# Kernel optimization log

Hardware: AMD Instinct MI355X
Metric: run time of the kernel (lower is better)

## Reference

```python
import jax, jax.numpy as jnp
import numpy as np

N, E = 20000, 320000
EPS = 1e-5
NEG_SLOPE = 0.2


def gat_conv(x, src, dst, W, att_src, att_dst, bias, num_nodes):
    # W: [Fin, H*C], att_*: [H, C], bias: [H*C]
    H, C = att_src.shape
    h = (x @ W).reshape(num_nodes, H, C)            # [N,H,C]
    a_s = jnp.einsum('nhc,hc->nh', h, att_src)      # [N,H]
    a_d = jnp.einsum('nhc,hc->nh', h, att_dst)      # [N,H]
    e = jax.nn.leaky_relu(a_s[src] + a_d[dst], NEG_SLOPE)  # [E,H]
    m = jax.ops.segment_max(e, dst, num_segments=num_nodes)       # per-dst max (self-loops guarantee non-empty)
    ex = jnp.exp(e - m[dst])
    s = jax.ops.segment_sum(ex, dst, num_segments=num_nodes)
    alpha = ex / s[dst]                              # [E,H] segment softmax
    out = jax.ops.segment_sum(h[src] * alpha[:, :, None], dst, num_segments=num_nodes)  # [N,H,C]
    return out.reshape(num_nodes, H * C) + bias


def batch_norm(x, gamma, beta):
    mu = x.mean(axis=0)
    var = x.var(axis=0)  # biased, as torch BN uses for normalization
    return (x - mu) * jax.lax.rsqrt(var + EPS) * gamma + beta


def setup_inputs() -> dict:
    key = jax.random.key(0)
    ks = jax.random.split(key, 32)
    x = jax.random.normal(ks[0], (N, 512), dtype=jnp.float32)
    edge_index = jax.random.randint(ks[1], (2, E), 0, N, dtype=jnp.int32)
    d = {"x": x, "edge_index": edge_index}
    # layer configs: (Fin, C_out, H)
    cfgs = [(512, 64, 8), (512, 64, 4), (256, 64, 2), (128, 16, 1)]
    i = 2
    for li, (fin, c, h) in enumerate(cfgs, start=1):
        sc = 1.0 / np.sqrt(fin)
        d[f"W{li}"] = jax.random.normal(ks[i], (fin, h * c), dtype=jnp.float32) * sc; i += 1
        d[f"as{li}"] = jax.random.normal(ks[i], (h, c), dtype=jnp.float32) * 0.1; i += 1
        d[f"ad{li}"] = jax.random.normal(ks[i], (h, c), dtype=jnp.float32) * 0.1; i += 1
        d[f"b{li}"] = jnp.zeros((h * c,), dtype=jnp.float32)
        if li < 4:
            d[f"g{li}"] = jnp.ones((h * c,), dtype=jnp.float32)
            d[f"be{li}"] = jnp.zeros((h * c,), dtype=jnp.float32)
    return d


def reference(x, edge_index, W1, as1, ad1, b1, g1, be1, W2, as2, ad2, b2, g2, be2, W3, as3, ad3, b3, g3, be3, W4, as4, ad4, b4):
    num_nodes = x.shape[0]
    loop = jnp.arange(num_nodes, dtype=edge_index.dtype)
    src = jnp.concatenate([edge_index[0], loop])  # add_self_loops=True
    dst = jnp.concatenate([edge_index[1], loop])
    h = gat_conv(x, src, dst, W1, as1, ad1, b1, num_nodes)
    h = jax.nn.elu(batch_norm(h, g1, be1))
    h = gat_conv(h, src, dst, W2, as2, ad2, b2, num_nodes)
    h = jax.nn.elu(batch_norm(h, g2, be2))
    h = gat_conv(h, src, dst, W3, as3, ad3, b3, num_nodes)
    h = jax.nn.elu(batch_norm(h, g3, be3))
    h = gat_conv(h, src, dst, W4, as4, ad4, b4, num_nodes)
    return jax.nn.log_softmax(h, axis=1)
```

## Files before the change

### kernel.cpp

```cpp
#include <hip/hip_runtime.h>
#include <hip/hip_bf16.h>
#include <cstdint>
#include <cstddef>

#define NN 20000
#define EE 320000
#define ET (EE + NN)
#define MPAD 20096
#define BNP 256

typedef __attribute__((ext_vector_type(8))) short  short8;
typedef __attribute__((ext_vector_type(4))) float  floatx4;

__device__ inline unsigned short f2bf(float f) {
    unsigned u = __float_as_uint(f);
    u += 0x7FFFu + ((u >> 16) & 1u);
    return (unsigned short)(u >> 16);
}
__device__ inline float bf2f(unsigned short b) {
    return __uint_as_float(((unsigned)b) << 16);
}
__device__ inline float bflo(unsigned u) { return __uint_as_float(u << 16); }
__device__ inline float bfhi(unsigned u) { return __uint_as_float(u & 0xFFFF0000u); }

template <int H> struct VecT;
template <> struct VecT<8> { using T = uint4; };
template <> struct VecT<4> { using T = uint2; };
template <> struct VecT<2> { using T = unsigned; };

__global__ void zero_i32(int* __restrict__ p, int n) {
    int i = blockIdx.x * blockDim.x + threadIdx.x;
    if (i < n) p[i] = 0;
}

__global__ void cvt_a_bf16(const float* __restrict__ in, unsigned short* __restrict__ out,
                           int M, int Mpad, int K) {
    long long base = ((long long)blockIdx.x * blockDim.x + threadIdx.x) * 4;
    if (base >= (long long)Mpad * K) return;
    int row = (int)(base / K);
    float4 v = make_float4(0.f, 0.f, 0.f, 0.f);
    if (row < M) v = *(const float4*)(in + base);
    ushort4 o;
    o.x = f2bf(v.x); o.y = f2bf(v.y); o.z = f2bf(v.z); o.w = f2bf(v.w);
    *(ushort4*)(out + base) = o;
}

__global__ void cvt_w_t(const float* __restrict__ W, unsigned short* __restrict__ Wt,
                        int K, int N) {
    int i = blockIdx.x * blockDim.x + threadIdx.x;
    if (i >= K * N) return;
    int k = i / N, n = i - k * N;
    Wt[(size_t)n * K + k] = f2bf(W[i]);
}

__global__ void count_edges(const int* __restrict__ dst, int* __restrict__ cnt) {
    int e = blockIdx.x * blockDim.x + threadIdx.x;
    if (e >= ET) return;
    int d = (e < EE) ? dst[e] : (e - EE);
    atomicAdd(&cnt[d], 1);
}

__global__ void scan20k(const int* __restrict__ cnt, int* __restrict__ rowp,
                        int* __restrict__ wptr, int n) {
    __shared__ int sd[1024];
    __shared__ int run;
    int t = threadIdx.x;
    if (t == 0) run = 0;
    __syncthreads();
    for (int base = 0; base < n; base += 1024) {
        int i = base + t;
        int v = (i < n) ? cnt[i] : 0;
        sd[t] = v;
        __syncthreads();
        for (int o = 1; o < 1024; o <<= 1) {
            int u = (t >= o) ? sd[t - o] : 0;
            __syncthreads();
            sd[t] += u;
            __syncthreads();
        }
        int incl = sd[t];
        int excl = incl - v;
        if (i < n) { int rp = run + excl; rowp[i] = rp; wptr[i] = rp; }
        __syncthreads();
        if (t == 1023) run += sd[1023];
        __syncthreads();
    }
    if (t == 0) rowp[n] = run;
}

__global__ void fill_edges(const int* __restrict__ src, const int* __restrict__ dst,
                           int* __restrict__ wptr, int* __restrict__ colx) {
    int e = blockIdx.x * blockDim.x + threadIdx.x;
    if (e >= ET) return;
    int s, d;
    if (e < EE) { s = src[e]; d = dst[e]; } else { s = e - EE; d = e - EE; }
    int pos = atomicAdd(&wptr[d], 1);
    colx[pos] = s;
}

__global__ __launch_bounds__(256) void gemm_bf16_fused(
        const unsigned short* __restrict__ A, const unsigned short* __restrict__ Bt,
        unsigned short* __restrict__ hN, float* __restrict__ aS, float* __restrict__ aD,
        const float* __restrict__ atts, const float* __restrict__ attd,
        int M, int N, int K) {
    __shared__ unsigned short As[128][40];
    __shared__ unsigned short Bs[128][40];
    const int t = threadIdx.x;
    const int lane = t & 63, wave = t >> 6;
    const int wm = wave >> 1, wn = wave & 1;
    const int quad = lane >> 4, mrow = lane & 15;
    const int row0 = blockIdx.y * 128, col0 = blockIdx.x * 128;
    const int srow = t >> 2, schunk = (t & 3) * 8;
    const int H = N >> 6;

    floatx4 acc[4][4];
#pragma unroll
    for (int i = 0; i < 4; ++i)
#pragma unroll
        for (int j = 0; j < 4; ++j)
#pragma unroll
            for (int r = 0; r < 4; ++r) acc[i][j][r] = 0.f;

    for (int k0 = 0; k0 < K; k0 += 32) {
        uint4 ra0 = *(const uint4*)(A  + (size_t)(row0 + srow)      * K + k0 + schunk);
        uint4 ra1 = *(const uint4*)(A  + (size_t)(row0 + srow + 64) * K + k0 + schunk);
        uint4 rb0 = *(const uint4*)(Bt + (size_t)(col0 + srow)      * K + k0 + schunk);
        uint4 rb1 = *(const uint4*)(Bt + (size_t)(col0 + srow + 64) * K + k0 + schunk);
        __syncthreads();
        *(uint4*)&As[srow][schunk]      = ra0;
        *(uint4*)&As[srow + 64][schunk] = ra1;
        *(uint4*)&Bs[srow][schunk]      = rb0;
        *(uint4*)&Bs[srow + 64][schunk] = rb1;
        __syncthreads();

        short8 af[4], bfr[4];
#pragma unroll
        for (int i = 0; i < 4; ++i)
            af[i] = *(const short8*)&As[wm * 64 + i * 16 + mrow][quad * 8];
#pragma unroll
        for (int j = 0; j < 4; ++j)
            bfr[j] = *(const short8*)&Bs[wn * 64 + j * 16 + mrow][quad * 8];
#pragma unroll
        for (int i = 0; i < 4; ++i)
#pragma unroll
            for (int j = 0; j < 4; ++j)
                acc[i][j] = __builtin_amdgcn_mfma_f32_16x16x32_bf16(af[i], bfr[j], acc[i][j], 0, 0, 0);
    }

    const int head = (col0 + wn * 64) >> 6;
    float attS[4], attD[4];
#pragma unroll
    for (int j = 0; j < 4; ++j) {
        attS[j] = atts[head * 64 + j * 16 + mrow];
        attD[j] = attd[head * 64 + j * 16 + mrow];
    }

#pragma unroll
    for (int i = 0; i < 4; ++i) {
#pragma unroll
        for (int r = 0; r < 4; ++r) {
            int row = row0 + wm * 64 + i * 16 + quad * 4 + r;
            float ps = acc[i][0][r] * attS[0] + acc[i][1][r] * attS[1]
                     + acc[i][2][r] * attS[2] + acc[i][3][r] * attS[3];
            float pd = acc[i][0][r] * attD[0] + acc[i][1][r] * attD[1]
                     + acc[i][2][r] * attD[2] + acc[i][3][r] * attD[3];
#pragma unroll
            for (int o = 1; o < 16; o <<= 1) {
                ps += __shfl_xor(ps, o);
                pd += __shfl_xor(pd, o);
            }
            if (row < M) {
                if (mrow == 0) {
                    aS[(size_t)row * H + head] = ps;
                    aD[(size_t)row * H + head] = pd;
                }
#pragma unroll
                for (int j = 0; j < 4; ++j)
                    hN[(size_t)row * N + col0 + wn * 64 + j * 16 + mrow] = f2bf(acc[i][j][r]);
            }
        }
    }
}

template <int H>
__global__ __launch_bounds__(256) void gat_agg_all(
        const unsigned short* __restrict__ hN,
        const float* __restrict__ aS, const float* __restrict__ aD,
        const int* __restrict__ rowp, const int* __restrict__ colx,
        const float* __restrict__ bias, float* __restrict__ out, int Nn) {
    constexpr int F = H * 64;
    using V = typename VecT<H>::T;
    __shared__ float pbuf[4][64 * H];
    __shared__ int   snbuf[4][64];
    const int wave = threadIdx.x >> 6, lane = threadIdx.x & 63;
    const int n = blockIdx.x * 4 + wave;
    if (n >= Nn) return;
    const int hd = (lane * H) >> 6;
    const int chbase = lane * H;

    const int b0 = rowp[n], b1 = rowp[n + 1];

    float adv[H];
#pragma unroll
    for (int h = 0; h < H; ++h) adv[h] = aD[(size_t)n * H + h];

    float m[H], s[H];
#pragma unroll
    for (int h = 0; h < H; ++h) { m[h] = -1e30f; s[h] = 0.f; }
    for (int c0 = b0; c0 < b1; c0 += 64) {
        int cnt = min(64, b1 - c0);
        float e[H];
#pragma unroll
        for (int h = 0; h < H; ++h) e[h] = -1e30f;
        if (lane < cnt) {
            int sn = colx[c0 + lane];
#pragma unroll
            for (int h = 0; h < H; ++h) {
                float tt = aS[(size_t)sn * H + h] + adv[h];
                e[h] = (tt > 0.f) ? tt : 0.2f * tt;
            }
        }
#pragma unroll
        for (int h = 0; h < H; ++h) {
            float mc = e[h];
#pragma unroll
            for (int o = 32; o > 0; o >>= 1) mc = fmaxf(mc, __shfl_xor(mc, o));
            float nm = fmaxf(m[h], mc);
            s[h] *= __expf(m[h] - nm);
            float p = (lane < cnt) ? __expf(e[h] - nm) : 0.f;
#pragma unroll
            for (int o = 32; o > 0; o >>= 1) p += __shfl_xor(p, o);
            s[h] += p; m[h] = nm;
        }
    }
    float inv[H];
#pragma unroll
    for (int h = 0; h < H; ++h) inv[h] = 1.f / s[h];

    float acc[H];
#pragma unroll
    for (int h = 0; h < H; ++h) acc[h] = 0.f;

    for (int c0 = b0; c0 < b1; c0 += 64) {
        int cnt = min(64, b1 - c0);
        if (lane < cnt) {
            int sn = colx[c0 + lane];
            snbuf[wave][lane] = sn;
#pragma unroll
            for (int h = 0; h < H; ++h) {
                float tt = aS[(size_t)sn * H + h] + adv[h];
                tt = (tt > 0.f) ? tt : 0.2f * tt;
                pbuf[wave][lane * H + h] = __expf(tt - m[h]) * inv[h];
            }
        }
        __threadfence_block();

        int j = 0;
        for (; j + 4 <= cnt; j += 4) {
            int s0 = snbuf[wave][j],     s1 = snbuf[wave][j + 1];
            int s2 = snbuf[wave][j + 2], s3 = snbuf[wave][j + 3];
            float p0 = pbuf[wave][(j + 0) * H + hd];
            float p1 = pbuf[wave][(j + 1) * H + hd];
            float p2 = pbuf[wave][(j + 2) * H + hd];
            float p3 = pbuf[wave][(j + 3) * H + hd];
            V q0 = *(const V*)(hN + (size_t)s0 * F + chbase);
            V q1 = *(const V*)(hN + (size_t)s1 * F + chbase);
            V q2 = *(const V*)(hN + (size_t)s2 * F + chbase);
            V q3 = *(const V*)(hN + (size_t)s3 * F + chbase);
            const unsigned* u0 = (const unsigned*)&q0;
            const unsigned* u1 = (const unsigned*)&q1;
            const unsigned* u2 = (const unsigned*)&q2;
            const unsigned* u3 = (const unsigned*)&q3;
#pragma unroll
            for (int k = 0; k < H / 2; ++k) {
                acc[2 * k]     += p0 * bflo(u0[k]) + p1 * bflo(u1[k]) + p2 * bflo(u2[k]) + p3 * bflo(u3[k]);
                acc[2 * k + 1] += p0 * bfhi(u0[k]) + p1 * bfhi(u1[k]) + p2 * bfhi(u2[k]) + p3 * bfhi(u3[k]);
            }
        }
        for (; j < cnt; ++j) {
            int sj = snbuf[wave][j];
            float pj = pbuf[wave][j * H + hd];
            V q = *(const V*)(hN + (size_t)sj * F + chbase);
            const unsigned* u = (const unsigned*)&q;
#pragma unroll
            for (int k = 0; k < H / 2; ++k) {
                acc[2 * k]     += pj * bflo(u[k]);
                acc[2 * k + 1] += pj * bfhi(u[k]);
            }
        }
        __threadfence_block();
    }

#pragma unroll
    for (int h = 0; h < H; ++h)
        out[(size_t)n * F + chbase + h] = acc[h] + bias[chbase + h];
}

__global__ __launch_bounds__(256) void gemm_l4_fused(const unsigned short* __restrict__ A,
                                                     const float* __restrict__ B,
                                                     unsigned short* __restrict__ C,
                                                     float* __restrict__ aS, float* __restrict__ aD,
                                                     const float* __restrict__ atts,
                                                     const float* __restrict__ attd,
                                                     int M, int N, int K) {
    __shared__ float As[16][65];
    __shared__ float Bs[16][64];
    const int tid = threadIdx.x;
    const int tx = tid & 15, ty = tid >> 4;
    const int row0 = blockIdx.y * 64, col0 = blockIdx.x * 64;
    const int rA = tid >> 2, kq = (tid & 3) << 2;
    const int rB = tid >> 4, cq = (tid & 15) << 2;
    float acc[4][4] = {};

    for (int k0 = 0; k0 < K; k0 += 16) {
        ushort4 ha = *(const ushort4*)(A + (size_t)(row0 + rA) * K + k0 + kq);
        float4 fb = make_float4(0.f, 0.f, 0.f, 0.f);
        int bcol = col0 + cq;
        if (bcol < N) fb = *(const float4*)(B + (size_t)(k0 + rB) * N + bcol);
        As[kq + 0][rA] = bf2f(ha.x); As[kq + 1][rA] = bf2f(ha.y);
        As[kq + 2][rA] = bf2f(ha.z); As[kq + 3][rA] = bf2f(ha.w);
        *(float4*)&Bs[rB][cq] = fb;
        __syncthreads();
#pragma unroll
        for (int k = 0; k < 16; ++k) {
            float a0 = As[k][ty * 4 + 0];
            float a1 = As[k][ty * 4 + 1];
            float a2 = As[k][ty * 4 + 2];
            float a3 = As[k][ty * 4 + 3];
            float4 b = *(float4*)&Bs[k][tx * 4];
            acc[0][0] += a0 * b.x; acc[0][1] += a0 * b.y; acc[0][2] += a0 * b.z; acc[0][3] += a0 * b.w;
            acc[1][0] += a1 * b.x; acc[1][1] += a1 * b.y; acc[1][2] += a1 * b.z; acc[1][3] += a1 * b.w;
            acc[2][0] += a2 * b.x; acc[2][1] += a2 * b.y; acc[2][2] += a2 * b.z; acc[2][3] += a2 * b.w;
            acc[3][0] += a3 * b.x; acc[3][1] += a3 * b.y; acc[3][2] += a3 * b.z; acc[3][3] += a3 * b.w;
        }
        __syncthreads();
    }
    float as_part[4], ad_part[4];
#pragma unroll
    for (int i = 0; i < 4; ++i) { as_part[i] = 0.f; ad_part[i] = 0.f; }
    if (tx < 4) {
#pragma unroll
        for (int i = 0; i < 4; ++i) {
#pragma unroll
            for (int jj = 0; jj < 4; ++jj) {
                int c = tx * 4 + jj;
                as_part[i] += acc[i][jj] * atts[c];
                ad_part[i] += acc[i][jj] * attd[c];
            }
        }
    }
#pragma unroll
    for (int i = 0; i < 4; ++i) {
        float ps = as_part[i], pd = ad_part[i];
        ps += __shfl_xor(ps, 1); ps += __shfl_xor(ps, 2);
        pd += __shfl_xor(pd, 1); pd += __shfl_xor(pd, 2);
        int r = row0 + ty * 4 + i;
        if (r < M) {
            if (tx == 0) { aS[r] = ps; aD[r] = pd; }
#pragma unroll
            for (int jj = 0; jj < 4; ++jj) {
                int c = col0 + tx * 4 + jj;
                if (c < N) C[(size_t)r * N + c] = f2bf(acc[i][jj]);
            }
        }
    }
}

template <int C>
__global__ void gat_agg_l4_ls(const unsigned short* __restrict__ ht,
                              const float* __restrict__ as, const float* __restrict__ aD,
                              const int* __restrict__ rowp, const int* __restrict__ colx,
                              const float* __restrict__ bias, float* __restrict__ out, int Nn) {
    int n = blockIdx.x * 4 + (threadIdx.x >> 6);
    int lane = threadIdx.x & 63;
    if (n >= Nn) return;
    float adv = aD[n];
    int b0 = rowp[n], b1 = rowp[n + 1];

    float m = -1e30f, s = 0.f, acc = 0.f;
    for (int c0 = b0; c0 < b1; c0 += 64) {
        int cnt = b1 - c0; if (cnt > 64) cnt = 64;
        int sn = 0; float e = -1e30f;
        if (lane < cnt) {
            sn = colx[c0 + lane];
            float tt = as[sn] + adv;
            e = (tt > 0.f) ? tt : 0.2f * tt;
        }
        float mc = e;
#pragma unroll
        for (int o = 32; o > 0; o >>= 1) mc = fmaxf(mc, __shfl_xor(mc, o));
        float nm = fmaxf(m, mc);
        float sc = __expf(m - nm);
        acc *= sc; s *= sc;
        float p = (lane < cnt) ? __expf(e - nm) : 0.f;
        float ps = p;
#pragma unroll
        for (int o = 32; o > 0; o >>= 1) ps += __shfl_xor(ps, o);
        s += ps; m = nm;

        int j = 0;
        for (; j + 4 <= cnt; j += 4) {
            int s0 = __shfl(sn, j),     s1 = __shfl(sn, j + 1);
            int s2 = __shfl(sn, j + 2), s3 = __shfl(sn, j + 3);
            float p0 = __shfl(p, j),     p1 = __shfl(p, j + 1);
            float p2 = __shfl(p, j + 2), p3 = __shfl(p, j + 3);
            float h0 = 0.f, h1 = 0.f, h2 = 0.f, h3 = 0.f;
            if (lane < C) {
                h0 = bf2f(ht[(size_t)s0 * C + lane]);
                h1 = bf2f(ht[(size_t)s1 * C + lane]);
                h2 = bf2f(ht[(size_t)s2 * C + lane]);
                h3 = bf2f(ht[(size_t)s3 * C + lane]);
            }
            acc += p0 * h0 + p1 * h1 + p2 * h2 + p3 * h3;
        }
        for (; j < cnt; ++j) {
            int sj = __shfl(sn, j);
            float pj = __shfl(p, j);
            float hv = (lane < C) ? bf2f(ht[(size_t)sj * C + lane]) : 0.f;
            acc += pj * hv;
        }
    }
    float v = (lane < C) ? (acc / s + bias[lane]) : -1e30f;
    float mx = v;
#pragma unroll
    for (int o = 8; o > 0; o >>= 1) mx = fmaxf(mx, __shfl_xor(mx, o));
    float ex = (lane < C) ? __expf(v - mx) : 0.f;
#pragma unroll
    for (int o = 8; o > 0; o >>= 1) ex += __shfl_xor(ex, o);
    float l = __logf(ex) + mx;
    if (lane < C) out[(size_t)n * C + lane] = v - l;
}

template <int F>
__global__ __launch_bounds__(256) void bn_stats_det(const float* __restrict__ x,
                                                    float* __restrict__ part,
                                                    long long total) {
    constexpr int R  = 1024 / F;
    constexpr int NT = F / 4;
    __shared__ float sd[256 * 9];
    const int t = threadIdx.x;
    long long idx = ((long long)blockIdx.x * 256 + t) * 4;
    const long long stride = (long long)gridDim.x * 1024;
    float s0 = 0, s1 = 0, s2 = 0, s3 = 0, q0 = 0, q1 = 0, q2 = 0, q3 = 0;
    for (; idx < total; idx += stride) {
        float4 v = *(const float4*)(x + idx);
        s0 += v.x; q0 += v.x * v.x;
        s1 += v.y; q1 += v.y * v.y;
        s2 += v.z; q2 += v.z * v.z;
        s3 += v.w; q3 += v.w * v.w;
    }
    sd[t * 9 + 0] = s0; sd[t * 9 + 1] = s1; sd[t * 9 + 2] = s2; sd[t * 9 + 3] = s3;
    sd[t * 9 + 4] = q0; sd[t * 9 + 5] = q1; sd[t * 9 + 6] = q2; sd[t * 9 + 7] = q3;
    __syncthreads();
    if (t < NT) {
        float a[8];
#pragma unroll
        for (int k = 0; k < 8; ++k) a[k] = sd[t * 9 + k];
        for (int r = 1; r < R; ++r)
#pragma unroll
            for (int k = 0; k < 8; ++k) a[k] += sd[(t + r * NT) * 9 + k];
        int col = t * 4;
        float* pb = part + (size_t)blockIdx.x * 2 * F;
#pragma unroll
        for (int k = 0; k < 4; ++k) {
            pb[col + k]     = a[k];
            pb[F + col + k] = a[4 + k];
        }
    }
}

template <int F>
__global__ __launch_bounds__(256) void bn_reduce_par(const float* __restrict__ part,
                                                     const float* __restrict__ gamma,
                                                     const float* __restrict__ beta,
                                                     float* __restrict__ ss,
                                                     float invN) {
    __shared__ float sd[8][33];
    const int t = threadIdx.x;
    const int pr = t >> 5;
    const int tg = t & 31;
    const int c0 = blockIdx.x * 16;
    const int col = (tg < 16) ? (c0 + tg) : (F + c0 + (tg - 16));
    float a = 0.f;
    for (int p = pr; p < BNP; p += 8)
        a += part[(size_t)p * 2 * F + col];
    sd[pr][tg] = a;
    __syncthreads();
    if (pr == 0) {
        float tot = sd[0][tg];
#pragma unroll
        for (int r = 1; r < 8; ++r) tot += sd[r][tg];
        sd[0][tg] = tot;
    }
    __syncthreads();
    if (t < 16) {
        int c = c0 + t;
        float s = sd[0][t];
        float q = sd[0][16 + t];
        float mu = s * invN;
        float var = q * invN - mu * mu;
        float sc = gamma[c] * rsqrtf(var + 1e-5f);
        ss[c] = sc;
        ss[F + c] = beta[c] - mu * sc;
    }
}

__global__ void bn_apply_elu_bf16(const float* __restrict__ x, const float* __restrict__ ss,
                                  unsigned short* __restrict__ outA,
                                  int Nn, int F, int fmask) {
    long long idx4 = ((long long)blockIdx.x * blockDim.x + threadIdx.x) * 4;
    int row = (int)(idx4 / F);
    ushort4 o = make_ushort4(0, 0, 0, 0);
    if (row < Nn) {
        int c = (int)(idx4 & fmask);
        float4 v = *(const float4*)(x + idx4);
        float v0 = v.x * ss[c + 0] + ss[F + c + 0];
        float v1 = v.y * ss[c + 1] + ss[F + c + 1];
        float v2 = v.z * ss[c + 2] + ss[F + c + 2];
        float v3 = v.w * ss[c + 3] + ss[F + c + 3];
        v0 = (v0 > 0.f) ? v0 : (__expf(v0) - 1.f);
        v1 = (v1 > 0.f) ? v1 : (__expf(v1) - 1.f);
        v2 = (v2 > 0.f) ? v2 : (__expf(v2) - 1.f);
        v3 = (v3 > 0.f) ? v3 : (__expf(v3) - 1.f);
        o.x = f2bf(v0); o.y = f2bf(v1); o.z = f2bf(v2); o.w = f2bf(v3);
    }
    *(ushort4*)(outA + idx4) = o;
}

extern "C" void kernel_launch(void* const* d_in, const int* in_sizes, int n_in,
                              void* d_out, int out_size, void* d_ws, size_t ws_size,
                              hipStream_t stream) {
    const float* x   = (const float*)d_in[0];
    const int*   ei  = (const int*)d_in[1];
    const float* W1  = (const float*)d_in[2];
    const float* as1 = (const float*)d_in[3];
    const float* ad1 = (const float*)d_in[4];
    const float* b1  = (const float*)d_in[5];
    const float* ga1 = (const float*)d_in[6];
    const float* be1 = (const float*)d_in[7];
    const float* W2  = (const float*)d_in[8];
    const float* as2 = (const float*)d_in[9];
    const float* ad2 = (const float*)d_in[10];
    const float* b2  = (const float*)d_in[11];
    const float* ga2 = (const float*)d_in[12];
    const float* be2 = (const float*)d_in[13];
    const float* W3  = (const float*)d_in[14];
    const float* as3 = (const float*)d_in[15];
    const float* ad3 = (const float*)d_in[16];
    const float* b3  = (const float*)d_in[17];
    const float* ga3 = (const float*)d_in[18];
    const float* be3 = (const float*)d_in[19];
    const float* W4  = (const float*)d_in[20];
    const float* as4 = (const float*)d_in[21];
    const float* ad4 = (const float*)d_in[22];
    const float* b4  = (const float*)d_in[23];
    float* outp = (float*)d_out;

    uint8_t* base = (uint8_t*)d_ws;
    size_t off = 0;
    auto alloc = [&](size_t nbytes) -> void* {
        off = (off + 255) & ~(size_t)255;
        void* p = base + off;
        off += nbytes;
        return p;
    };
    float* bufO = (float*)alloc((size_t)NN * 512 * 4);
    unsigned short* bufA = (unsigned short*)alloc((size_t)MPAD * 512 * 2);
    unsigned short* hN   = (unsigned short*)alloc((size_t)NN * 512 * 2);
    unsigned short* Wt1  = (unsigned short*)alloc((size_t)512 * 512 * 2);
    unsigned short* Wt2  = (unsigned short*)alloc((size_t)256 * 512 * 2);
    unsigned short* Wt3  = (unsigned short*)alloc((size_t)128 * 256 * 2);
    float* aSn  = (float*)alloc((size_t)NN * 8 * 4);
    float* aDn  = (float*)alloc((size_t)NN * 8 * 4);
    int*   cnt  = (int*)alloc((size_t)NN * 4);
    int*   rowp = (int*)alloc((size_t)(NN + 1) * 4);
    int*   wptr = (int*)alloc((size_t)NN * 4);
    int*   colx = (int*)alloc((size_t)ET * 4);
    float* bnp  = (float*)alloc((size_t)BNP * 1024 * 4);
    float* bns  = (float*)alloc((size_t)1024 * 4);

    const int* srcRow = ei;
    const int* dstRow = ei + EE;

    zero_i32<<<(NN + 255) / 256, 256, 0, stream>>>(cnt, NN);
    count_edges<<<(ET + 255) / 256, 256, 0, stream>>>(dstRow, cnt);
    scan20k<<<1, 1024, 0, stream>>>(cnt, rowp, wptr, NN);
    fill_edges<<<(ET + 255) / 256, 256, 0, stream>>>(srcRow, dstRow, wptr, colx);

    cvt_w_t<<<(512 * 512 + 255) / 256, 256, 0, stream>>>(W1, Wt1, 512, 512);
    cvt_w_t<<<(512 * 256 + 255) / 256, 256, 0, stream>>>(W2, Wt2, 512, 256);
    cvt_w_t<<<(256 * 128 + 255) / 256, 256, 0, stream>>>(W3, Wt3, 256, 128);

    {
        cvt_a_bf16<<<((MPAD * 512 / 4) + 255) / 256, 256, 0, stream>>>(x, bufA, NN, MPAD, 512);
        dim3 g(512 / 128, MPAD / 128);
        gemm_bf16_fused<<<g, 256, 0, stream>>>(bufA, Wt1, hN, aSn, aDn, as1, ad1, NN, 512, 512);
        gat_agg_all<8><<<NN / 4, 256, 0, stream>>>(hN, aSn, aDn, rowp, colx, b1, bufO, NN);
        bn_stats_det<512><<<BNP, 256, 0, stream>>>(bufO, bnp, (long long)NN * 512);
        bn_reduce_par<512><<<512 / 16, 256, 0, stream>>>(bnp, ga1, be1, bns, 1.0f / NN);
        bn_apply_elu_bf16<<<(MPAD * 512 / 4) / 256, 256, 0, stream>>>(bufO, bns, bufA, NN, 512, 511);
    }
    {
        dim3 g(256 / 128, MPAD / 128);
        gemm_bf16_fused<<<g, 256, 0, stream>>>(bufA, Wt2, hN, aSn, aDn, as2, ad2, NN, 256, 512);
        gat_agg_all<4><<<NN / 4, 256, 0, stream>>>(hN, aSn, aDn, rowp, colx, b2, bufO, NN);
        bn_stats_det<256><<<BNP, 256, 0, stream>>>(bufO, bnp, (long long)NN * 256);
        bn_reduce_par<256><<<256 / 16, 256, 0, stream>>>(bnp, ga2, be2, bns, 1.0f / NN);
        bn_apply_elu_bf16<<<(MPAD * 256 / 4) / 256, 256, 0, stream>>>(bufO, bns, bufA, NN, 256, 255);
    }
    {
        dim3 g(128 / 128, MPAD / 128);
        gemm_bf16_fused<<<g, 256, 0, stream>>>(bufA, Wt3, hN, aSn, aDn, as3, ad3, NN, 128, 256);
        gat_agg_all<2><<<NN / 4, 256, 0, stream>>>(hN, aSn, aDn, rowp, colx, b3, bufO, NN);
        bn_stats_det<128><<<BNP, 256, 0, stream>>>(bufO, bnp, (long long)NN * 128);
        bn_reduce_par<128><<<128 / 16, 256, 0, stream>>>(bnp, ga3, be3, bns, 1.0f / NN);
        bn_apply_elu_bf16<<<(MPAD * 128 / 4) / 256, 256, 0, stream>>>(bufO, bns, bufA, NN, 128, 127);
    }
    {
        dim3 g(1, (NN + 63) / 64);
        gemm_l4_fused<<<g, 256, 0, stream>>>(bufA, W4, hN, aSn, aDn, as4, ad4, NN, 16, 128);
        gat_agg_l4_ls<16><<<(NN + 3) / 4, 256, 0, stream>>>(hN, aSn, aDn, rowp, colx, b4, outp, NN);
    }
}
```

Measured before the change: 477.6 us.

## Single-pass softmax for low-degree nodes and chunked single-block scan

The aggregation kernel gains a fast path for nodes with at most 64 incoming edges. It computes the max, the exp-sum and the normalized weights in one pass, avoiding the second reload of colx and aS and the recomputation of exp. The row-pointer scan is also rewritten so each of 1024 threads scans 20 consecutive counts serially before a single block-wide scan, instead of 20 sequential block scans. The cost is duplicated aggregation code and more register pressure from the two branches.

```diff
diff --git a/kernel.cpp b/kernel.cpp
--- a/kernel.cpp
+++ b/kernel.cpp
@@ -8,6 +8,7 @@
 #define ET (EE + NN)
 #define MPAD 20096
 #define BNP 256
+#define SCHUNK 20
 
 typedef __attribute__((ext_vector_type(8))) short  short8;
 typedef __attribute__((ext_vector_type(4))) float  floatx4;
@@ -60,32 +61,36 @@
     atomicAdd(&cnt[d], 1);
 }
 
-__global__ void scan20k(const int* __restrict__ cnt, int* __restrict__ rowp,
-                        int* __restrict__ wptr, int n) {
-    __shared__ int sd[1024];
-    __shared__ int run;
-    int t = threadIdx.x;
-    if (t == 0) run = 0;
+__global__ __launch_bounds__(1024) void scan_fast(const int* __restrict__ cnt,
+                                                  int* __restrict__ rowp,
+                                                  int* __restrict__ wptr, int n) {
+    __shared__ int sums[1024];
+    const int t = threadIdx.x;
+    const int base = t * SCHUNK;
+    int local[SCHUNK];
+    int acc = 0;
+#pragma unroll
+    for (int i = 0; i < SCHUNK; ++i) {
+        int idx = base + i;
+        int v = (idx < n) ? cnt[idx] : 0;
+        local[i] = acc;
+        acc += v;
+    }
+    sums[t] = acc;
     __syncthreads();
-    for (int base = 0; base < n; base += 1024) {
-        int i = base + t;
-        int v = (i < n) ? cnt[i] : 0;
-        sd[t] = v;
+    for (int o = 1; o < 1024; o <<= 1) {
+        int u = (t >= o) ? sums[t - o] : 0;
         __syncthreads();
-        for (int o = 1; o < 1024; o <<= 1) {
-            int u = (t >= o) ? sd[t - o] : 0;
-            __syncthreads();
-            sd[t] += u;
-            __syncthreads();
-        }
-        int incl = sd[t];
-        int excl = incl - v;
-        if (i < n) { int rp = run + excl; rowp[i] = rp; wptr[i] = rp; }
+        sums[t] += u;
         __syncthreads();
-        if (t == 1023) run += sd[1023];
-        __syncthreads();
-    }
-    if (t == 0) rowp[n] = run;
+    }
+    int excl = sums[t] - acc;
+#pragma unroll
+    for (int i = 0; i < SCHUNK; ++i) {
+        int idx = base + i;
+        if (idx < n) { int rp = excl + local[i]; rowp[idx] = rp; wptr[idx] = rp; }
+    }
+    if (t == 1023) rowp[n] = sums[1023];
 }
 
 __global__ void fill_edges(const int* __restrict__ src, const int* __restrict__ dst,
@@ -199,21 +204,24 @@
     const int chbase = lane * H;
 
     const int b0 = rowp[n], b1 = rowp[n + 1];
+    const int deg = b1 - b0;
 
     float adv[H];
 #pragma unroll
     for (int h = 0; h < H; ++h) adv[h] = aD[(size_t)n * H + h];
 
-    float m[H], s[H];
-#pragma unroll
-    for (int h = 0; h < H; ++h) { m[h] = -1e30f; s[h] = 0.f; }
-    for (int c0 = b0; c0 < b1; c0 += 64) {
-        int cnt = min(64, b1 - c0);
+    float acc[H];
+#pragma unroll
+    for (int h = 0; h < H; ++h) acc[h] = 0.f;
+
+    if (deg <= 64) {
+        const int cnt = deg;
         float e[H];
 #pragma unroll
         for (int h = 0; h < H; ++h) e[h] = -1e30f;
         if (lane < cnt) {
-            int sn = colx[c0 + lane];
+            int sn = colx[b0 + lane];
+            snbuf[wave][lane] = sn;
 #pragma unroll
             for (int h = 0; h < H; ++h) {
                 float tt = aS[(size_t)sn * H + h] + adv[h];
@@ -225,33 +233,11 @@
             float mc = e[h];
 #pragma unroll
             for (int o = 32; o > 0; o >>= 1) mc = fmaxf(mc, __shfl_xor(mc, o));
-            float nm = fmaxf(m[h], mc);
-            s[h] *= __expf(m[h] - nm);
-            float p = (lane < cnt) ? __expf(e[h] - nm) : 0.f;
-#pragma unroll
-            for (int o = 32; o > 0; o >>= 1) p += __shfl_xor(p, o);
-            s[h] += p; m[h] = nm;
-        }
-    }
-    float inv[H];
-#pragma unroll
-    for (int h = 0; h < H; ++h) inv[h] = 1.f / s[h];
-
-    float acc[H];
-#pragma unroll
-    for (int h = 0; h < H; ++h) acc[h] = 0.f;
-
-    for (int c0 = b0; c0 < b1; c0 += 64) {
-        int cnt = min(64, b1 - c0);
-        if (lane < cnt) {
-            int sn = colx[c0 + lane];
-            snbuf[wave][lane] = sn;
-#pragma unroll
-            for (int h = 0; h < H; ++h) {
-                float tt = aS[(size_t)sn * H + h] + adv[h];
-                tt = (tt > 0.f) ? tt : 0.2f * tt;
-                pbuf[wave][lane * H + h] = __expf(tt - m[h]) * inv[h];
-            }
+            float p = (lane < cnt) ? __expf(e[h] - mc) : 0.f;
+            float ps = p;
+#pragma unroll
+            for (int o = 32; o > 0; o >>= 1) ps += __shfl_xor(ps, o);
+            if (lane < cnt) pbuf[wave][lane * H + h] = p / ps;
         }
         __threadfence_block();
 
@@ -288,7 +274,89 @@
                 acc[2 * k + 1] += pj * bfhi(u[k]);
             }
         }
-        __threadfence_block();
+    } else {
+        float m[H], s[H];
+#pragma unroll
+        for (int h = 0; h < H; ++h) { m[h] = -1e30f; s[h] = 0.f; }
+        for (int c0 = b0; c0 < b1; c0 += 64) {
+            int cnt = min(64, b1 - c0);
+            float e[H];
+#pragma unroll
+            for (int h = 0; h < H; ++h) e[h] = -1e30f;
+            if (lane < cnt) {
+                int sn = colx[c0 + lane];
+#pragma unroll
+                for (int h = 0; h < H; ++h) {
+                    float tt = aS[(size_t)sn * H + h] + adv[h];
+                    e[h] = (tt > 0.f) ? tt : 0.2f * tt;
+                }
+            }
+#pragma unroll
+            for (int h = 0; h < H; ++h) {
+                float mc = e[h];
+#pragma unroll
+                for (int o = 32; o > 0; o >>= 1) mc = fmaxf(mc, __shfl_xor(mc, o));
+                float nm = fmaxf(m[h], mc);
+                s[h] *= __expf(m[h] - nm);
+                float p = (lane < cnt) ? __expf(e[h] - nm) : 0.f;
+#pragma unroll
+                for (int o = 32; o > 0; o >>= 1) p += __shfl_xor(p, o);
+                s[h] += p; m[h] = nm;
+            }
+        }
+        float inv[H];
+#pragma unroll
+        for (int h = 0; h < H; ++h) inv[h] = 1.f / s[h];
+
+        for (int c0 = b0; c0 < b1; c0 += 64) {
+            int cnt = min(64, b1 - c0);
+            if (lane < cnt) {
+                int sn = colx[c0 + lane];
+                snbuf[wave][lane] = sn;
+#pragma unroll
+                for (int h = 0; h < H; ++h) {
+                    float tt = aS[(size_t)sn * H + h] + adv[h];
+                    tt = (tt > 0.f) ? tt : 0.2f * tt;
+                    pbuf[wave][lane * H + h] = __expf(tt - m[h]) * inv[h];
+                }
+            }
+            __threadfence_block();
+
+            int j = 0;
+            for (; j + 4 <= cnt; j += 4) {
+                int s0 = snbuf[wave][j],     s1 = snbuf[wave][j + 1];
+                int s2 = snbuf[wave][j + 2], s3 = snbuf[wave][j + 3];
+                float p0 = pbuf[wave][(j + 0) * H + hd];
+                float p1 = pbuf[wave][(j + 1) * H + hd];
+                float p2 = pbuf[wave][(j + 2) * H + hd];
+                float p3 = pbuf[wave][(j + 3) * H + hd];
+                V q0 = *(const V*)(hN + (size_t)s0 * F + chbase);
+                V q1 = *(const V*)(hN + (size_t)s1 * F + chbase);
+                V q2 = *(const V*)(hN + (size_t)s2 * F + chbase);
+                V q3 = *(const V*)(hN + (size_t)s3 * F + chbase);
+                const unsigned* u0 = (const unsigned*)&q0;
+                const unsigned* u1 = (const unsigned*)&q1;
+                const unsigned* u2 = (const unsigned*)&q2;
+                const unsigned* u3 = (const unsigned*)&q3;
+#pragma unroll
+                for (int k = 0; k < H / 2; ++k) {
+                    acc[2 * k]     += p0 * bflo(u0[k]) + p1 * bflo(u1[k]) + p2 * bflo(u2[k]) + p3 * bflo(u3[k]);
+                    acc[2 * k + 1] += p0 * bfhi(u0[k]) + p1 * bfhi(u1[k]) + p2 * bfhi(u2[k]) + p3 * bfhi(u3[k]);
+                }
+            }
+            for (; j < cnt; ++j) {
+                int sj = snbuf[wave][j];
+                float pj = pbuf[wave][j * H + hd];
+                V q = *(const V*)(hN + (size_t)sj * F + chbase);
+                const unsigned* u = (const unsigned*)&q;
+#pragma unroll
+                for (int k = 0; k < H / 2; ++k) {
+                    acc[2 * k]     += pj * bflo(u[k]);
+                    acc[2 * k + 1] += pj * bfhi(u[k]);
+                }
+            }
+            __threadfence_block();
+        }
     }
 
 #pragma unroll
@@ -584,7 +652,7 @@
 
     zero_i32<<<(NN + 255) / 256, 256, 0, stream>>>(cnt, NN);
     count_edges<<<(ET + 255) / 256, 256, 0, stream>>>(dstRow, cnt);
-    scan20k<<<1, 1024, 0, stream>>>(cnt, rowp, wptr, NN);
+    scan_fast<<<1, 1024, 0, stream>>>(cnt, rowp, wptr, NN);
     fill_edges<<<(ET + 255) / 256, 256, 0, stream>>>(srcRow, dstRow, wptr, colx);
 
     cvt_w_t<<<(512 * 512 + 255) / 256, 256, 0, stream>>>(W1, Wt1, 512, 512);
```

Measured after the change: 480.2 us. About the same (+0.6%).
